# Kernel tuning notes

Hardware: AMD Instinct MI355X
Metric: run time of the kernel (lower is better)

## Reference

```python
import jax, jax.numpy as jnp
import numpy as np

EPS = 1e-5
NEG = -10000.0


def rel_shift(x):
    # x: [B, H, T1, T2] with T2 = 2*T1 - 1 -> returns [B, H, T1, T1]
    B, H, T1, T2 = x.shape
    x = jnp.pad(x, ((0, 0), (0, 0), (0, 0), (1, 0)))        # [B,H,T1,T2+1]
    x = x.reshape(B, H, T2 + 1, T1)[:, :, 1:, :].reshape(B, H, T1, T2)
    return x[:, :, :, : T2 // 2 + 1]


def setup_inputs() -> dict:
    key = jax.random.key(0)
    B, C, T, H = 4, 512, 1024, 8
    ks = jax.random.split(key, 16)
    s = 0.02
    inp = {
        "x": jax.random.normal(ks[0], (B, C, T), jnp.float32),
        "pos_emb": jax.random.normal(ks[1], (1, C, 2 * T - 1), jnp.float32),
        "x_mask": jnp.ones((B, 1, T), jnp.float32),
        "gamma": jnp.ones((C,), jnp.float32),
        "beta": jnp.zeros((C,), jnp.float32),
        "Wq": jax.random.normal(ks[2], (C, C), jnp.float32) * s,
        "bq": jnp.zeros((C,), jnp.float32),
        "Wk": jax.random.normal(ks[3], (C, C), jnp.float32) * s,
        "bk": jnp.zeros((C,), jnp.float32),
        "Wv": jax.random.normal(ks[4], (C, C), jnp.float32) * s,
        "bv": jnp.zeros((C,), jnp.float32),
        "Wp": jax.random.normal(ks[5], (C, C), jnp.float32) * s,
        "u_bias": jax.random.normal(ks[6], (H, C // H), jnp.float32) * s,
        "v_bias": jax.random.normal(ks[7], (H, C // H), jnp.float32) * s,
        "Wo": jax.random.normal(ks[8], (C, C), jnp.float32) * s,
        "bo": jnp.zeros((C,), jnp.float32),
    }
    return inp


def reference(x, pos_emb, x_mask, gamma, beta, Wq, bq, Wk, bk, Wv, bv, Wp,
              u_bias, v_bias, Wo, bo):
    B, C, T = x.shape
    H, Dh = u_bias.shape

    # channel LayerNorm (axis=1)
    mean = jnp.mean(x, axis=1, keepdims=True)
    var = jnp.mean((x - mean) ** 2, axis=1, keepdims=True)
    xn = (x - mean) * jax.lax.rsqrt(var + EPS)
    xn = xn * gamma[None, :, None] + beta[None, :, None]

    conv1x1 = lambda W, b, z: jnp.einsum('oc,bct->bot', W, z) + b[None, :, None]
    q = conv1x1(Wq, bq, xn).reshape(B, H, Dh, T)
    k = conv1x1(Wk, bk, xn).reshape(B, H, Dh, T)
    v = conv1x1(Wv, bv, xn).reshape(B, H, Dh, T)
    p = jnp.einsum('oc,xct->xot', Wp, pos_emb)          # [1, C, 2T-1], no bias
    p = p.reshape(p.shape[0], H, Dh, -1)[0]             # [H, Dh, 2T-1]

    content = jnp.einsum('bhdt,bhds->bhts', q + u_bias[None, :, :, None], k)
    pos = jnp.einsum('bhdt,hds->bhts', q + v_bias[None, :, :, None], p)
    pos = rel_shift(pos)                                 # [B, H, T, T]

    score = (content + pos) / jnp.sqrt(jnp.float32(C))
    attn_mask = x_mask[:, :, None, :] * x_mask[:, :, :, None]  # [B,1,T,T]
    score = jnp.where(attn_mask == 0, NEG, score)
    attn = jax.nn.softmax(score, axis=-1)

    # context[d,t] = sum_s v[d,s] * attn[s,t]
    ctx = jnp.einsum('bhds,bhst->bhdt', v, attn).reshape(B, C, T)
    return jnp.einsum('oc,bct->bot', Wo, ctx) + bo[None, :, None]
```

## Files before the change

kernel.cpp:

```cpp
#include <hip/hip_runtime.h>
#include <hip/hip_bf16.h>
#include <cmath>

typedef unsigned short u16;
typedef __bf16 bf16_t;
typedef bf16_t bf16x8 __attribute__((ext_vector_type(8)));
typedef bf16_t bf16x2 __attribute__((ext_vector_type(2)));
typedef float f32x4 __attribute__((ext_vector_type(4)));
typedef u16 u16x8 __attribute__((ext_vector_type(8)));

#define MFMA16(A,B,C) __builtin_amdgcn_mfma_f32_16x16x32_bf16(A,B,C,0,0,0)

#define CB 512
#define TT 1024
#define NH 8
#define DH 64
#define ALPHA (0.044194173824159216f * 1.4426950408889634f)
#define MASKL 14426.950408889634f

static __device__ __forceinline__ u16 f2b(float f) {
  union { bf16_t b; u16 u; } r; r.b = (bf16_t)f; return r.u;
}
static __device__ __forceinline__ unsigned cvt2(float lo, float hi) {
  union { bf16x2 v; unsigned u; } r;
  r.v[0] = (bf16_t)lo; r.v[1] = (bf16_t)hi; return r.u;
}
static __device__ __forceinline__ float b2f(u16 u) {
  return __uint_as_float(((unsigned)u) << 16);
}
static __device__ __forceinline__ bf16x8 ldb8(const u16* p) {
  return *reinterpret_cast<const bf16x8*>(p);
}

__global__ __launch_bounds__(256)
void prefix_kernel(const float* __restrict__ Wq, const float* __restrict__ Wk,
                   const float* __restrict__ Wv, const float* __restrict__ Wp,
                   const float* __restrict__ Wo,
                   u16* __restrict__ Wstk, u16* __restrict__ WoB,
                   const float* __restrict__ pe, u16* __restrict__ posT,
                   const float* __restrict__ x, const float* __restrict__ gamma,
                   const float* __restrict__ beta, u16* __restrict__ xnT)
{
  __shared__ float tile[64][65];
  const int bid = blockIdx.x;
  const int tid = threadIdx.x;
  if (bid < 640) {
    int i = bid * 256 + tid;
    int sel = i >> 15, loc = i & 32767;
    const float* src = (sel == 0) ? Wq : (sel == 1) ? Wk : (sel == 2) ? Wv
                     : (sel == 3) ? Wp : Wo;
    const float4 a = ((const float4*)src)[loc * 2 + 0];
    const float4 b = ((const float4*)src)[loc * 2 + 1];
    u16x8 o;
    o[0] = f2b(a.x); o[1] = f2b(a.y); o[2] = f2b(a.z); o[3] = f2b(a.w);
    o[4] = f2b(b.x); o[5] = f2b(b.y); o[6] = f2b(b.z); o[7] = f2b(b.w);
    u16* dst = (sel < 4) ? (Wstk + (size_t)i * 8) : (WoB + (size_t)loc * 8);
    *(u16x8*)dst = o;
  } else if (bid < 896) {
    int bb = bid - 640;
    int j0 = (bb & 31) * 64, c0 = (bb >> 5) * 64;
    for (int e = tid; e < 4096; e += 256) {
      int cc = e >> 6, jj = e & 63;
      int j = j0 + jj;
      tile[jj][cc] = (j < 2047) ? pe[(size_t)(c0 + cc) * 2047 + j] : 0.f;
    }
    __syncthreads();
    for (int e = tid; e < 4096; e += 256) {
      int jj = e >> 6, cc = e & 63;
      posT[(size_t)(j0 + jj) * 512 + c0 + cc] = f2b(tile[jj][cc]);
    }
  } else {
    float (*sred)[33]  = (float(*)[33])&tile[0][0];
    float (*ssred)[33] = (float(*)[33])&tile[8][0];
    int bb = bid - 896;
    int tl = tid & 31, cg = tid >> 5;
    int t = (bb & 31) * 32 + tl;
    int b = bb >> 5;
    const float* xb = x + (size_t)b * CB * TT + t;
    float s = 0.f, ss = 0.f;
    for (int c = cg * 64; c < cg * 64 + 64; ++c) {
      float v = xb[(size_t)c * TT];
      s += v; ss += v * v;
    }
    sred[cg][tl] = s; ssred[cg][tl] = ss;
    __syncthreads();
    float S = 0.f, SS = 0.f;
    #pragma unroll
    for (int g = 0; g < 8; ++g) { S += sred[g][tl]; SS += ssred[g][tl]; }
    float mean = S * (1.f / 512.f);
    float var = SS * (1.f / 512.f) - mean * mean;
    float rstd = rsqrtf(var + 1e-5f);
    u16* orow = xnT + ((size_t)b * TT + t) * CB;
    for (int c8 = 0; c8 < 8; ++c8) {
      int c = cg * 64 + c8 * 8;
      u16x8 o;
      #pragma unroll
      for (int j = 0; j < 8; ++j) {
        float v = xb[(size_t)(c + j) * TT];
        o[j] = f2b((v - mean) * rstd * gamma[c + j] + beta[c + j]);
      }
      *(u16x8*)(orow + c) = o;
    }
  }
}

__global__ __launch_bounds__(256)
void proj_kernel(const u16* __restrict__ Wstk, const u16* __restrict__ xnT,
                 const u16* __restrict__ posT,
                 const float* __restrict__ bq, const float* __restrict__ ub,
                 const float* __restrict__ bk, const float* __restrict__ bv,
                 u16* __restrict__ quB, u16* __restrict__ kB, u16* __restrict__ vB,
                 u16* __restrict__ pB)
{
  const int bid = blockIdx.x;
  const int tid = threadIdx.x, w = tid >> 6, lane = tid & 63;
  const int ln16 = lane & 15, kg = lane >> 4;
  if (bid < 768) {
    const int bx = bid & 7;
    const int t = bid >> 3;
    const int my = t % 24;
    const int z = t / 24;
    const int wm = w & 1, wn = w >> 1;
    const int sec = my >> 3;
    const int m0l = (my & 7) * 64 + wm * 32;
    const int n0 = bx * 128 + wn * 64;
    const long XS = (long)TT * CB;
    const long QS = (long)NH * TT * DH;
    const u16* Ar = Wstk + (size_t)(sec * 512 + m0l + ln16) * 512 + kg * 8;
    const u16* Br = xnT + (size_t)z * XS + (size_t)(n0 + ln16) * 512 + kg * 8;
    f32x4 acc[2][4] = {};
    #pragma unroll 2
    for (int ks = 0; ks < 16; ++ks) {
      bf16x8 a[2], bb[4];
      #pragma unroll
      for (int mt = 0; mt < 2; ++mt) a[mt] = ldb8(Ar + (size_t)mt * 16 * 512 + ks * 32);
      #pragma unroll
      for (int nt = 0; nt < 4; ++nt) bb[nt] = ldb8(Br + (size_t)nt * 16 * 512 + ks * 32);
      #pragma unroll
      for (int mt = 0; mt < 2; ++mt)
        #pragma unroll
        for (int nt = 0; nt < 4; ++nt)
          acc[mt][nt] = MFMA16(a[mt], bb[nt], acc[mt][nt]);
    }
    const float scl = (sec == 0) ? ALPHA : 1.f;
    float add[2][4];
    #pragma unroll
    for (int mt = 0; mt < 2; ++mt)
      #pragma unroll
      for (int jr = 0; jr < 4; ++jr) {
        int m = m0l + mt * 16 + kg * 4 + jr;
        add[mt][jr] = (sec == 0) ? (bq[m] + ub[m]) : (sec == 1) ? bk[m] : bv[m];
      }
    if (sec < 2) {
      u16* dst = sec ? kB : quB;
      #pragma unroll
      for (int mt = 0; mt < 2; ++mt)
        #pragma unroll
        for (int nt = 0; nt < 4; ++nt) {
          const int n = n0 + nt * 16 + ln16;
          const int m_low = m0l + mt * 16;
          const size_t o = (size_t)z * QS +
                           ((size_t)(m_low >> 6) * TT + n) * 64 + (m_low & 63) + kg * 4;
          uint2 o2;
          o2.x = cvt2((acc[mt][nt][0] + add[mt][0]) * scl,
                      (acc[mt][nt][1] + add[mt][1]) * scl);
          o2.y = cvt2((acc[mt][nt][2] + add[mt][2]) * scl,
                      (acc[mt][nt][3] + add[mt][3]) * scl);
          *reinterpret_cast<uint2*>(dst + o) = o2;
        }
    } else {
      #pragma unroll
      for (int mt = 0; mt < 2; ++mt)
        #pragma unroll
        for (int nt = 0; nt < 4; ++nt) {
          const int n = n0 + nt * 16 + ln16;
          #pragma unroll
          for (int jr = 0; jr < 4; ++jr)
            vB[(size_t)z * QS + (size_t)(m0l + mt * 16 + kg * 4 + jr) * TT + n] =
                f2b(acc[mt][nt][jr] + add[mt][jr]);
        }
    }
  } else {
    const int i = bid - 768;
    const int m0 = (i >> 5) * 64 + (w & 1) * 32;
    const int n0 = (i & 31) * 64 + (w >> 1) * 32;
    const u16* Ar = Wstk + (size_t)(1536 + m0 + ln16) * 512 + kg * 8;
    const u16* Br = posT + (size_t)(n0 + ln16) * 512 + kg * 8;
    f32x4 acc[2][2] = {};
    #pragma unroll 2
    for (int ks = 0; ks < 16; ++ks) {
      bf16x8 a[2], bb[2];
      #pragma unroll
      for (int mt = 0; mt < 2; ++mt) a[mt] = ldb8(Ar + (size_t)mt * 16 * 512 + ks * 32);
      #pragma unroll
      for (int nt = 0; nt < 2; ++nt) bb[nt] = ldb8(Br + (size_t)nt * 16 * 512 + ks * 32);
      #pragma unroll
      for (int mt = 0; mt < 2; ++mt)
        #pragma unroll
        for (int nt = 0; nt < 2; ++nt)
          acc[mt][nt] = MFMA16(a[mt], bb[nt], acc[mt][nt]);
    }
    #pragma unroll
    for (int mt = 0; mt < 2; ++mt)
      #pragma unroll
      for (int nt = 0; nt < 2; ++nt) {
        const int n = n0 + nt * 16 + ln16;
        const int m_low = m0 + mt * 16;
        const size_t o = ((size_t)(m_low >> 6) * 2048 + n) * 64 + (m_low & 63) + kg * 4;
        uint2 o2;
        o2.x = cvt2(acc[mt][nt][0], acc[mt][nt][1]);
        o2.y = cvt2(acc[mt][nt][2], acc[mt][nt][3]);
        *reinterpret_cast<uint2*>(pB + o) = o2;
      }
  }
}

template<int K, int OMODE>
__global__ __launch_bounds__(256)
void gemm2(const u16* __restrict__ A, const u16* __restrict__ XT,
           long xStride, long oStride, int Nout,
           const float* __restrict__ b0, void* __restrict__ outv)
{
  const int tid = threadIdx.x, w = tid >> 6, lane = tid & 63;
  const int ln16 = lane & 15, kg = lane >> 4;
  const int wm = w & 1, wn = w >> 1;
  const int m0 = blockIdx.y * 64 + wm * 32;
  const int n0 = blockIdx.x * 128 + wn * 64;
  const int z = blockIdx.z;
  const u16* Ar = A + (size_t)(m0 + ln16) * K + kg * 8;
  const u16* Br = XT + (size_t)z * xStride + (size_t)(n0 + ln16) * K + kg * 8;
  f32x4 acc[2][4] = {};
  #pragma unroll 2
  for (int ks = 0; ks < K / 32; ++ks) {
    bf16x8 a[2], bb[4];
    #pragma unroll
    for (int mt = 0; mt < 2; ++mt) a[mt] = ldb8(Ar + (size_t)mt * 16 * K + ks * 32);
    #pragma unroll
    for (int nt = 0; nt < 4; ++nt) bb[nt] = ldb8(Br + (size_t)nt * 16 * K + ks * 32);
    #pragma unroll
    for (int mt = 0; mt < 2; ++mt)
      #pragma unroll
      for (int nt = 0; nt < 4; ++nt)
        acc[mt][nt] = MFMA16(a[mt], bb[nt], acc[mt][nt]);
  }
  float add[2][4];
  #pragma unroll
  for (int mt = 0; mt < 2; ++mt)
    #pragma unroll
    for (int jr = 0; jr < 4; ++jr)
      add[mt][jr] = b0 ? b0[m0 + mt * 16 + kg * 4 + jr] : 0.f;
  #pragma unroll
  for (int mt = 0; mt < 2; ++mt)
    #pragma unroll
    for (int nt = 0; nt < 4; ++nt) {
      const int n = n0 + nt * 16 + ln16;
      if constexpr (OMODE == 0) {
        float* out = (float*)outv;
        #pragma unroll
        for (int jr = 0; jr < 4; ++jr)
          out[(size_t)z * oStride + (size_t)(m0 + mt * 16 + kg * 4 + jr) * Nout + n] =
              acc[mt][nt][jr] + add[mt][jr];
      } else {
        const int m_low = m0 + mt * 16;
        const size_t o = (size_t)z * oStride +
                         ((size_t)(m_low >> 6) * Nout + n) * 64 + (m_low & 63) + kg * 4;
        uint2 o2;
        o2.x = cvt2(acc[mt][nt][0] + add[mt][0], acc[mt][nt][1] + add[mt][1]);
        o2.y = cvt2(acc[mt][nt][2] + add[mt][2], acc[mt][nt][3] + add[mt][3]);
        *reinterpret_cast<uint2*>((u16*)outv + o) = o2;
      }
    }
}

__global__ __launch_bounds__(256)
void corr_kernel(const u16* __restrict__ pp, const float* __restrict__ ub,
                 const float* __restrict__ vb, float* __restrict__ corr)
{
  const int h = blockIdx.y;
  const int j = blockIdx.x * 256 + threadIdx.x;
  __shared__ float dl[64];
  if (threadIdx.x < 64)
    dl[threadIdx.x] = vb[h * 64 + threadIdx.x] - ub[h * 64 + threadIdx.x];
  __syncthreads();
  const u16* prow = pp + ((size_t)h * 2048 + j) * 64;
  float s = 0.f;
  #pragma unroll
  for (int d8 = 0; d8 < 8; ++d8) {
    union { bf16x8 v; u16 u[8]; } pu;
    pu.v = ldb8(prow + d8 * 8);
    #pragma unroll
    for (int e = 0; e < 8; ++e) s += b2f(pu.u[e]) * dl[d8 * 8 + e];
  }
  corr[h * 2048 + j] = s * ALPHA;
}

__global__ __launch_bounds__(256)
void stats_mfma(const u16* __restrict__ qu, const u16* __restrict__ kk_,
                const u16* __restrict__ pp, const float* __restrict__ corr,
                const float* __restrict__ xmask, float* __restrict__ ls)
{
  const int tid = threadIdx.x;
  const int w = tid >> 6, lane = tid & 63;
  const int ln16 = lane & 15, kg = lane >> 4;
  const int bid = blockIdx.x;
  const int bh = (bid & 7) + 8 * ((bid >> 3) & 3);
  const int rest = bid >> 5;
  const int qi0 = (rest & 31) * 32;
  const int part = rest >> 5;
  const int b = bh >> 3, h = bh & 7;
  const u16* quP = qu + (size_t)bh * TT * DH;
  const u16* kP  = kk_ + (size_t)bh * TT * DH;
  const u16* pP  = pp + (size_t)h * 2048 * DH;
  const float* corrP = corr + (h << 11);

  __shared__ u16 G[4][32][100];
  __shared__ float red[4][32];

  bf16x8 qa[2][2];
  #pragma unroll
  for (int mt = 0; mt < 2; ++mt)
    #pragma unroll
    for (int kc = 0; kc < 2; ++kc)
      qa[mt][kc] = ldb8(&quP[(size_t)(qi0 + mt * 16 + ln16) * DH + kc * 32 + kg * 8]);
  float aq[2][4];
  #pragma unroll
  for (int mt = 0; mt < 2; ++mt)
    #pragma unroll
    for (int jr = 0; jr < 4; ++jr)
      aq[mt][jr] = (xmask[b * TT + qi0 + mt * 16 + kg * 4 + jr] - 1.f) * MASKL;

  float rs[2][4] = {};
  for (int c = 0; c < 2; ++c) {
    const int ki0 = (part * 8 + c * 4 + w) * 64;
    const int j0 = ki0 - qi0 + 992;
    #pragma unroll
    for (int nt = 0; nt < 6; ++nt) {
      const size_t po = (size_t)(j0 + nt * 16 + ln16) * DH + kg * 8;
      bf16x8 pb0 = ldb8(&pP[po]);
      bf16x8 pb1 = ldb8(&pP[po + 32]);
      const float cval = corrP[j0 + nt * 16 + ln16];
      #pragma unroll
      for (int mt = 0; mt < 2; ++mt) {
        f32x4 g = {0.f, 0.f, 0.f, 0.f};
        g = MFMA16(qa[mt][0], pb0, g);
        g = MFMA16(qa[mt][1], pb1, g);
        #pragma unroll
        for (int jr = 0; jr < 4; ++jr)
          G[w][mt * 16 + kg * 4 + jr][nt * 16 + ln16] = f2b(g[jr] + cval);
      }
    }
    #pragma unroll
    for (int nt = 0; nt < 4; ++nt) {
      const size_t ko = (size_t)(ki0 + nt * 16 + ln16) * DH + kg * 8;
      bf16x8 kb0 = ldb8(&kP[ko]);
      bf16x8 kb1 = ldb8(&kP[ko + 32]);
      const float ak = (xmask[b * TT + ki0 + nt * 16 + ln16] - 1.f) * MASKL;
      #pragma unroll
      for (int mt = 0; mt < 2; ++mt) {
        f32x4 dd = { aq[mt][0] + ak, aq[mt][1] + ak, aq[mt][2] + ak, aq[mt][3] + ak };
        dd = MFMA16(qa[mt][0], kb0, dd);
        dd = MFMA16(qa[mt][1], kb1, dd);
        #pragma unroll
        for (int jr = 0; jr < 4; ++jr) {
          const int qrow = mt * 16 + kg * 4 + jr;
          const int u = nt * 16 + ln16 - qrow + 31;
          rs[mt][jr] += exp2f(dd[jr] + b2f(G[w][qrow][u]));
        }
      }
    }
  }
  #pragma unroll
  for (int mt = 0; mt < 2; ++mt)
    #pragma unroll
    for (int jr = 0; jr < 4; ++jr) {
      float v = rs[mt][jr];
      v += __shfl_xor(v, 1); v += __shfl_xor(v, 2);
      v += __shfl_xor(v, 4); v += __shfl_xor(v, 8);
      rs[mt][jr] = v;
    }
  if (ln16 == 0) {
    #pragma unroll
    for (int mt = 0; mt < 2; ++mt)
      #pragma unroll
      for (int jr = 0; jr < 4; ++jr)
        red[w][mt * 16 + kg * 4 + jr] = rs[mt][jr];
  }
  __syncthreads();
  if (tid < 32)
    ls[(size_t)part * 32768 + (size_t)bh * TT + qi0 + tid] =
        red[0][tid] + red[1][tid] + red[2][tid] + red[3][tid];
}

__global__ __launch_bounds__(256)
void ctx_mfma(const u16* __restrict__ qu, const u16* __restrict__ kk_,
              const u16* __restrict__ vv, const u16* __restrict__ pp,
              const float* __restrict__ corr, const float* __restrict__ xmask,
              u16* __restrict__ ctx2)
{
  const int tid = threadIdx.x;
  const int w = tid >> 6, lane = tid & 63;
  const int ln16 = lane & 15, kg = lane >> 4;
  const int l48 = lane & 48;
  const int bid = blockIdx.x;
  const int bh = (bid & 7) + 8 * ((bid >> 3) & 3);
  const int rest = bid >> 5;
  const int t0 = (rest & 15) * 64;
  const int part = rest >> 4;
  const int b = bh >> 3, h = bh & 7;
  const u16* quP = qu + (size_t)bh * TT * DH;
  const u16* kP  = kk_ + (size_t)bh * TT * DH;
  const u16* vP  = vv + (size_t)bh * DH * TT;
  const u16* pP  = pp + (size_t)h * 2048 * DH;
  const float* corrP = corr + (h << 11);

  __shared__ __align__(16) u16 P[2][64][72];

  bf16x8 ka[4][2];
  #pragma unroll
  for (int nt = 0; nt < 4; ++nt)
    #pragma unroll
    for (int kc = 0; kc < 2; ++kc)
      ka[nt][kc] = ldb8(&kP[(size_t)(t0 + nt * 16 + ln16) * DH + kc * 32 + kg * 8]);
  float at4[4];
  #pragma unroll
  for (int nt = 0; nt < 4; ++nt)
    at4[nt] = (xmask[b * TT + t0 + nt * 16 + ln16] - 1.f) * MASKL;

  auto scores = [&](int qcn, int buf) {
    const int qw = qcn * 64 + w * 16;
    const int j0 = t0 - qw + 1008;
    const size_t qo = (size_t)(qw + ln16) * DH + kg * 8;
    bf16x8 qa0 = ldb8(&quP[qo]), qa1 = ldb8(&quP[qo + 32]);
    f32x4 g[5];
    #pragma unroll
    for (int n = 0; n < 5; ++n) {
      const size_t po = (size_t)(j0 + n * 16 + ln16) * DH + kg * 8;
      bf16x8 pb0 = ldb8(&pP[po]), pb1 = ldb8(&pP[po + 32]);
      const float cval = corrP[j0 + n * 16 + ln16];
      f32x4 t = {cval, cval, cval, cval};
      t = MFMA16(qa0, pb0, t);
      t = MFMA16(qa1, pb1, t);
      g[n] = t;
    }
    float sg[4][5];
    #pragma unroll
    for (int jr = 0; jr < 4; ++jr) {
      const int qrow = kg * 4 + jr;
      const int src = l48 | ((ln16 + 15 - qrow) & 15);
      #pragma unroll
      for (int n = 0; n < 5; ++n) sg[jr][n] = __shfl(g[n][jr], src);
    }
    float aqv[4];
    #pragma unroll
    for (int jr = 0; jr < 4; ++jr)
      aqv[jr] = (xmask[b * TT + qw + kg * 4 + jr] - 1.f) * MASKL;
    #pragma unroll
    for (int nt = 0; nt < 4; ++nt) {
      f32x4 dd = { aqv[0] + at4[nt], aqv[1] + at4[nt],
                   aqv[2] + at4[nt], aqv[3] + at4[nt] };
      dd = MFMA16(qa0, ka[nt][0], dd);
      dd = MFMA16(qa1, ka[nt][1], dd);
      float ev[4];
      #pragma unroll
      for (int jr = 0; jr < 4; ++jr) {
        const int qrow = kg * 4 + jr;
        const float val = (ln16 <= qrow) ? sg[jr][nt] : sg[jr][nt + 1];
        ev[jr] = exp2f(dd[jr] + val);
      }
      uint2 o2;
      o2.x = cvt2(ev[0], ev[1]);
      o2.y = cvt2(ev[2], ev[3]);
      *reinterpret_cast<uint2*>(&P[buf][nt * 16 + ln16][w * 16 + kg * 4]) = o2;
    }
  };

  f32x4 cacc[4] = {};
  scores(part * 4, 0);
  __syncthreads();
  #pragma unroll
  for (int i = 0; i < 4; ++i) {
    const int qc = part * 4 + i;
    const size_t vbase = (size_t)(w * 16 + ln16) * TT + qc * 64 + kg * 8;
    bf16x8 vf0 = ldb8(&vP[vbase]), vf1 = ldb8(&vP[vbase + 32]);
    __builtin_amdgcn_s_setprio(1);
    #pragma unroll
    for (int nt = 0; nt < 4; ++nt) {
      bf16x8 pb0 = *reinterpret_cast<const bf16x8*>(&P[i & 1][nt * 16 + ln16][kg * 8]);
      bf16x8 pb1 = *reinterpret_cast<const bf16x8*>(&P[i & 1][nt * 16 + ln16][32 + kg * 8]);
      cacc[nt] = MFMA16(vf0, pb0, cacc[nt]);
      cacc[nt] = MFMA16(vf1, pb1, cacc[nt]);
    }
    __builtin_amdgcn_s_setprio(0);
    if (i < 3) {
      scores(qc + 1, (i + 1) & 1);
      __syncthreads();
    }
  }
  #pragma unroll
  for (int nt = 0; nt < 4; ++nt) {
    const int t = t0 + nt * 16 + ln16;
    uint2 o2;
    o2.x = cvt2(cacc[nt][0], cacc[nt][1]);
    o2.y = cvt2(cacc[nt][2], cacc[nt][3]);
    *reinterpret_cast<uint2*>(
      &ctx2[((size_t)b * TT + t) * 2048 + part * 512 + h * 64 + w * 16 + kg * 4]) = o2;
  }
}

__global__ __launch_bounds__(256)
void vscale(u16* __restrict__ vv, const float* __restrict__ ls)
{
  int i = blockIdx.x * 256 + threadIdx.x;
  int bh = i >> 13;
  int rem = i & 8191;
  int d = rem >> 7;
  int qi0 = (rem & 127) * 8;
  const float* lsP = ls + bh * 1024 + qi0;
  u16* row = vv + ((size_t)bh * 64 + d) * 1024 + qi0;
  union { u16x8 v; u16 u[8]; } t;
  t.v = *(u16x8*)row;
  u16x8 o;
  #pragma unroll
  for (int e = 0; e < 8; ++e) {
    float linv = __builtin_amdgcn_rcpf(lsP[e] + lsP[32768 + e]);
    o[e] = f2b(b2f(t.u[e]) * linv);
  }
  *(u16x8*)row = o;
}

__global__ __launch_bounds__(256)
void reduce_ctx(const u16* __restrict__ ctx2, u16* __restrict__ ctxS)
{
  int i = blockIdx.x * 256 + threadIdx.x;
  int row = i >> 6;
  int c0 = (i & 63) * 8;
  const u16* src = ctx2 + (size_t)row * 2048 + c0;
  float s[8] = {};
  #pragma unroll
  for (int p = 0; p < 4; ++p) {
    union { u16x8 v; u16 u[8]; } t;
    t.v = *(const u16x8*)(src + p * 512);
    #pragma unroll
    for (int e = 0; e < 8; ++e) s[e] += b2f(t.u[e]);
  }
  u16x8 o;
  #pragma unroll
  for (int e = 0; e < 8; ++e) o[e] = f2b(s[e]);
  *(u16x8*)(ctxS + (size_t)row * 512 + c0) = o;
}

extern "C" void kernel_launch(void* const* d_in, const int* in_sizes, int n_in,
                              void* d_out, int out_size, void* d_ws, size_t ws_size,
                              hipStream_t stream)
{
  (void)in_sizes; (void)n_in; (void)out_size;
  const float* x     = (const float*)d_in[0];
  const float* pe    = (const float*)d_in[1];
  const float* xm    = (const float*)d_in[2];
  const float* gamma = (const float*)d_in[3];
  const float* beta  = (const float*)d_in[4];
  const float* Wq    = (const float*)d_in[5];
  const float* bq    = (const float*)d_in[6];
  const float* Wk    = (const float*)d_in[7];
  const float* bk    = (const float*)d_in[8];
  const float* Wv    = (const float*)d_in[9];
  const float* bv    = (const float*)d_in[10];
  const float* Wp    = (const float*)d_in[11];
  const float* ub    = (const float*)d_in[12];
  const float* vb    = (const float*)d_in[13];
  const float* Wo    = (const float*)d_in[14];
  const float* bo    = (const float*)d_in[15];

  char* ws = (char*)d_ws;
  u16*  quB  = (u16*) (ws + 0);
  u16*  ctxS = (u16*) (ws + 0);
  u16*  kB   = (u16*) (ws + 4194304);
  u16*  vB   = (u16*) (ws + 8388608);
  u16*  pB   = (u16*) (ws + 12582912);
  float* corrB = (float*)(ws + 14680064);
  float* lsB = (float*)(ws + 14745600);
  u16*  WoB  = (u16*) (ws + 15007744);
  u16*  ctx2 = (u16*) (ws + 15532032);
  u16*  xnT  = (u16*) (ws + 15532032);
  u16*  posT = (u16*) (ws + 19726336);
  u16*  Wstk = (u16*) (ws + 21823488);
  if (ws_size < 32309248) return;

  dim3 blk(256);

  prefix_kernel<<<dim3(1024), blk, 0, stream>>>(
      Wq, Wk, Wv, Wp, Wo, Wstk, WoB, pe, posT, x, gamma, beta, xnT);
  proj_kernel<<<dim3(1024), blk, 0, stream>>>(
      Wstk, xnT, posT, bq, ub, bk, bv, quB, kB, vB, pB);
  corr_kernel<<<dim3(8, 8), blk, 0, stream>>>(pB, ub, vb, corrB);

  stats_mfma<<<dim3(2048), blk, 0, stream>>>(quB, kB, pB, corrB, xm, lsB);
  vscale<<<dim3(1024), blk, 0, stream>>>(vB, lsB);
  ctx_mfma<<<dim3(2048), blk, 0, stream>>>(quB, kB, vB, pB, corrB, xm, ctx2);
  reduce_ctx<<<dim3(1024), blk, 0, stream>>>(ctx2, ctxS);

  gemm2<512, 0><<<dim3(8, 8, 4), blk, 0, stream>>>(
      WoB, ctxS, (long)TT * CB, (long)CB * TT, TT, bo, (float*)d_out);
}
```

Before: 198.6 us.

## Fold corr kernel into prefix/proj and keep P in registers for ctx MFMA

The standalone corr kernel goes away. A new prefix block precomputes Wp^T(v_bias-u_bias) per head, and extra proj blocks dot posT rows with it to produce the correction vector, which saves one launch. ctx_mfma no longer stages exp scores through double-buffered LDS with barriers. Each wave feeds its score fragments straight into 16x16x16 MFMAs against V fragments for all 64 head dims, and the four waves' partial sums are reduced through LDS at the end. This trades per-chunk syncs for 4x more accumulators, a final cross-wave reduction and a changed rounding order of the correction term.

Result: slower. 229.1 us (+15.3%).

```diff
diff --git a/kernel.cpp b/kernel.cpp
--- a/kernel.cpp
+++ b/kernel.cpp
@@ -8,8 +8,10 @@
 typedef bf16_t bf16x2 __attribute__((ext_vector_type(2)));
 typedef float f32x4 __attribute__((ext_vector_type(4)));
 typedef u16 u16x8 __attribute__((ext_vector_type(8)));
+typedef short s16x4 __attribute__((ext_vector_type(4)));
 
 #define MFMA16(A,B,C) __builtin_amdgcn_mfma_f32_16x16x32_bf16(A,B,C,0,0,0)
+#define MFMA16K16(A,B,C) __builtin_amdgcn_mfma_f32_16x16x16bf16_1k(A,B,C,0,0,0)
 
 #define CB 512
 #define TT 1024
@@ -39,7 +41,9 @@
                    u16* __restrict__ Wstk, u16* __restrict__ WoB,
                    const float* __restrict__ pe, u16* __restrict__ posT,
                    const float* __restrict__ x, const float* __restrict__ gamma,
-                   const float* __restrict__ beta, u16* __restrict__ xnT)
+                   const float* __restrict__ beta, u16* __restrict__ xnT,
+                   const float* __restrict__ ub, const float* __restrict__ vb,
+                   float* __restrict__ wcorr)
 {
   __shared__ float tile[64][65];
   const int bid = blockIdx.x;
@@ -69,7 +73,7 @@
       int jj = e >> 6, cc = e & 63;
       posT[(size_t)(j0 + jj) * 512 + c0 + cc] = f2b(tile[jj][cc]);
     }
-  } else {
+  } else if (bid < 1024) {
     float (*sred)[33]  = (float(*)[33])&tile[0][0];
     float (*ssred)[33] = (float(*)[33])&tile[8][0];
     int bb = bid - 896;
@@ -101,6 +105,21 @@
       }
       *(u16x8*)(orow + c) = o;
     }
+  } else {
+    float* dl2 = &tile[0][0];
+    for (int i = tid; i < 512; i += 256) dl2[i] = vb[i] - ub[i];
+    __syncthreads();
+    const int hh = tid >> 5;
+    const int c0 = (tid & 31) * 16;
+    float acc[16] = {};
+    for (int d = 0; d < 64; ++d) {
+      const float dv = dl2[hh * 64 + d];
+      const float* wrow = Wp + (size_t)(hh * 64 + d) * 512 + c0;
+      #pragma unroll
+      for (int j = 0; j < 16; ++j) acc[j] += dv * wrow[j];
+    }
+    #pragma unroll
+    for (int j = 0; j < 16; ++j) wcorr[hh * 512 + c0 + j] = acc[j];
   }
 }
 
@@ -109,9 +128,11 @@
                  const u16* __restrict__ posT,
                  const float* __restrict__ bq, const float* __restrict__ ub,
                  const float* __restrict__ bk, const float* __restrict__ bv,
+                 const float* __restrict__ wcorr,
                  u16* __restrict__ quB, u16* __restrict__ kB, u16* __restrict__ vB,
-                 u16* __restrict__ pB)
-{
+                 u16* __restrict__ pB, float* __restrict__ corrOut)
+{
+  __shared__ float wc[512];
   const int bid = blockIdx.x;
   const int tid = threadIdx.x, w = tid >> 6, lane = tid & 63;
   const int ln16 = lane & 15, kg = lane >> 4;
@@ -180,7 +201,7 @@
                 f2b(acc[mt][nt][jr] + add[mt][jr]);
         }
     }
-  } else {
+  } else if (bid < 1024) {
     const int i = bid - 768;
     const int m0 = (i >> 5) * 64 + (w & 1) * 32;
     const int n0 = (i & 31) * 64 + (w >> 1) * 32;
@@ -212,6 +233,22 @@
         o2.y = cvt2(acc[mt][nt][2], acc[mt][nt][3]);
         *reinterpret_cast<uint2*>(pB + o) = o2;
       }
+  } else {
+    const int i = bid - 1024;
+    const int hh = i >> 3;
+    const int j = (i & 7) * 256 + tid;
+    for (int c = tid; c < 512; c += 256) wc[c] = wcorr[hh * 512 + c];
+    __syncthreads();
+    const u16* prow = posT + (size_t)j * 512;
+    float s = 0.f;
+    #pragma unroll 4
+    for (int c8 = 0; c8 < 64; ++c8) {
+      union { bf16x8 v; u16 u[8]; } pu;
+      pu.v = ldb8(prow + c8 * 8);
+      #pragma unroll
+      for (int e = 0; e < 8; ++e) s += b2f(pu.u[e]) * wc[c8 * 8 + e];
+    }
+    corrOut[hh * 2048 + j] = s * ALPHA;
   }
 }
 
@@ -270,28 +307,6 @@
         *reinterpret_cast<uint2*>((u16*)outv + o) = o2;
       }
     }
-}
-
-__global__ __launch_bounds__(256)
-void corr_kernel(const u16* __restrict__ pp, const float* __restrict__ ub,
-                 const float* __restrict__ vb, float* __restrict__ corr)
-{
-  const int h = blockIdx.y;
-  const int j = blockIdx.x * 256 + threadIdx.x;
-  __shared__ float dl[64];
-  if (threadIdx.x < 64)
-    dl[threadIdx.x] = vb[h * 64 + threadIdx.x] - ub[h * 64 + threadIdx.x];
-  __syncthreads();
-  const u16* prow = pp + ((size_t)h * 2048 + j) * 64;
-  float s = 0.f;
-  #pragma unroll
-  for (int d8 = 0; d8 < 8; ++d8) {
-    union { bf16x8 v; u16 u[8]; } pu;
-    pu.v = ldb8(prow + d8 * 8);
-    #pragma unroll
-    for (int e = 0; e < 8; ++e) s += b2f(pu.u[e]) * dl[d8 * 8 + e];
-  }
-  corr[h * 2048 + j] = s * ALPHA;
 }
 
 __global__ __launch_bounds__(256)
@@ -413,7 +428,7 @@
   const u16* pP  = pp + (size_t)h * 2048 * DH;
   const float* corrP = corr + (h << 11);
 
-  __shared__ __align__(16) u16 P[2][64][72];
+  __shared__ float buf[4][2][64][4][4];
 
   bf16x8 ka[4][2];
   #pragma unroll
@@ -426,29 +441,31 @@
   for (int nt = 0; nt < 4; ++nt)
     at4[nt] = (xmask[b * TT + t0 + nt * 16 + ln16] - 1.f) * MASKL;
 
-  auto scores = [&](int qcn, int buf) {
-    const int qw = qcn * 64 + w * 16;
+  f32x4 cacc[4][4] = {};
+  for (int qc = part * 4; qc < part * 4 + 4; ++qc) {
+    const int qw = qc * 64 + w * 16;
     const int j0 = t0 - qw + 1008;
     const size_t qo = (size_t)(qw + ln16) * DH + kg * 8;
     bf16x8 qa0 = ldb8(&quP[qo]), qa1 = ldb8(&quP[qo + 32]);
-    f32x4 g[5];
+    s16x4 vfr[4];
+    #pragma unroll
+    for (int df = 0; df < 4; ++df)
+      vfr[df] = *reinterpret_cast<const s16x4*>(
+          &vP[(size_t)(df * 16 + ln16) * TT + qw + kg * 4]);
+    float sg[4][5];
     #pragma unroll
     for (int n = 0; n < 5; ++n) {
       const size_t po = (size_t)(j0 + n * 16 + ln16) * DH + kg * 8;
       bf16x8 pb0 = ldb8(&pP[po]), pb1 = ldb8(&pP[po + 32]);
       const float cval = corrP[j0 + n * 16 + ln16];
-      f32x4 t = {cval, cval, cval, cval};
-      t = MFMA16(qa0, pb0, t);
-      t = MFMA16(qa1, pb1, t);
-      g[n] = t;
-    }
-    float sg[4][5];
-    #pragma unroll
-    for (int jr = 0; jr < 4; ++jr) {
-      const int qrow = kg * 4 + jr;
-      const int src = l48 | ((ln16 + 15 - qrow) & 15);
-      #pragma unroll
-      for (int n = 0; n < 5; ++n) sg[jr][n] = __shfl(g[n][jr], src);
+      f32x4 g = {cval, cval, cval, cval};
+      g = MFMA16(qa0, pb0, g);
+      g = MFMA16(qa1, pb1, g);
+      #pragma unroll
+      for (int jr = 0; jr < 4; ++jr) {
+        const int src = l48 | ((ln16 + 15 - (kg * 4 + jr)) & 15);
+        sg[jr][n] = __shfl(g[jr], src);
+      }
     }
     float aqv[4];
     #pragma unroll
@@ -467,43 +484,44 @@
         const float val = (ln16 <= qrow) ? sg[jr][nt] : sg[jr][nt + 1];
         ev[jr] = exp2f(dd[jr] + val);
       }
-      uint2 o2;
-      o2.x = cvt2(ev[0], ev[1]);
-      o2.y = cvt2(ev[2], ev[3]);
-      *reinterpret_cast<uint2*>(&P[buf][nt * 16 + ln16][w * 16 + kg * 4]) = o2;
-    }
-  };
-
-  f32x4 cacc[4] = {};
-  scores(part * 4, 0);
-  __syncthreads();
-  #pragma unroll
-  for (int i = 0; i < 4; ++i) {
-    const int qc = part * 4 + i;
-    const size_t vbase = (size_t)(w * 16 + ln16) * TT + qc * 64 + kg * 8;
-    bf16x8 vf0 = ldb8(&vP[vbase]), vf1 = ldb8(&vP[vbase + 32]);
-    __builtin_amdgcn_s_setprio(1);
-    #pragma unroll
-    for (int nt = 0; nt < 4; ++nt) {
-      bf16x8 pb0 = *reinterpret_cast<const bf16x8*>(&P[i & 1][nt * 16 + ln16][kg * 8]);
-      bf16x8 pb1 = *reinterpret_cast<const bf16x8*>(&P[i & 1][nt * 16 + ln16][32 + kg * 8]);
-      cacc[nt] = MFMA16(vf0, pb0, cacc[nt]);
-      cacc[nt] = MFMA16(vf1, pb1, cacc[nt]);
-    }
-    __builtin_amdgcn_s_setprio(0);
-    if (i < 3) {
-      scores(qc + 1, (i + 1) & 1);
-      __syncthreads();
-    }
-  }
-  #pragma unroll
-  for (int nt = 0; nt < 4; ++nt) {
-    const int t = t0 + nt * 16 + ln16;
-    uint2 o2;
-    o2.x = cvt2(cacc[nt][0], cacc[nt][1]);
-    o2.y = cvt2(cacc[nt][2], cacc[nt][3]);
-    *reinterpret_cast<uint2*>(
-      &ctx2[((size_t)b * TT + t) * 2048 + part * 512 + h * 64 + w * 16 + kg * 4]) = o2;
+      union { uint2 u; s16x4 s; } pa;
+      pa.u = make_uint2(cvt2(ev[0], ev[1]), cvt2(ev[2], ev[3]));
+      #pragma unroll
+      for (int df = 0; df < 4; ++df)
+        cacc[df][nt] = MFMA16K16(vfr[df], pa.s, cacc[df][nt]);
+    }
+  }
+  #pragma unroll
+  for (int r = 0; r < 2; ++r) {
+    if (r) __syncthreads();
+    #pragma unroll
+    for (int y = 0; y < 2; ++y)
+      #pragma unroll
+      for (int nt = 0; nt < 4; ++nt)
+        #pragma unroll
+        for (int jr = 0; jr < 4; ++jr)
+          buf[w][y][lane][nt][jr] = cacc[r * 2 + y][nt][jr];
+    __syncthreads();
+    if (w < 2) {
+      const int df = r * 2 + w;
+      #pragma unroll
+      for (int nt = 0; nt < 4; ++nt) {
+        float s0 = buf[0][w][lane][nt][0] + buf[1][w][lane][nt][0] +
+                   buf[2][w][lane][nt][0] + buf[3][w][lane][nt][0];
+        float s1 = buf[0][w][lane][nt][1] + buf[1][w][lane][nt][1] +
+                   buf[2][w][lane][nt][1] + buf[3][w][lane][nt][1];
+        float s2 = buf[0][w][lane][nt][2] + buf[1][w][lane][nt][2] +
+                   buf[2][w][lane][nt][2] + buf[3][w][lane][nt][2];
+        float s3 = buf[0][w][lane][nt][3] + buf[1][w][lane][nt][3] +
+                   buf[2][w][lane][nt][3] + buf[3][w][lane][nt][3];
+        const int t = t0 + nt * 16 + ln16;
+        uint2 o2;
+        o2.x = cvt2(s0, s1);
+        o2.y = cvt2(s2, s3);
+        *reinterpret_cast<uint2*>(
+          &ctx2[((size_t)b * TT + t) * 2048 + part * 512 + h * 64 + df * 16 + kg * 4]) = o2;
+      }
+    }
   }
 }
 
@@ -584,15 +602,15 @@
   u16*  xnT  = (u16*) (ws + 15532032);
   u16*  posT = (u16*) (ws + 19726336);
   u16*  Wstk = (u16*) (ws + 21823488);
+  float* wcorrB = (float*)(ws + 23920640);
   if (ws_size < 32309248) return;
 
   dim3 blk(256);
 
-  prefix_kernel<<<dim3(1024), blk, 0, stream>>>(
-      Wq, Wk, Wv, Wp, Wo, Wstk, WoB, pe, posT, x, gamma, beta, xnT);
-  proj_kernel<<<dim3(1024), blk, 0, stream>>>(
-      Wstk, xnT, posT, bq, ub, bk, bv, quB, kB, vB, pB);
-  corr_kernel<<<dim3(8, 8), blk, 0, stream>>>(pB, ub, vb, corrB);
+  prefix_kernel<<<dim3(1025), blk, 0, stream>>>(
+      Wq, Wk, Wv, Wp, Wo, Wstk, WoB, pe, posT, x, gamma, beta, xnT, ub, vb, wcorrB);
+  proj_kernel<<<dim3(1088), blk, 0, stream>>>(
+      Wstk, xnT, posT, bq, ub, bk, bv, wcorrB, quB, kB, vB, pB, corrB);
 
   stats_mfma<<<dim3(2048), blk, 0, stream>>>(quB, kB, pB, corrB, xm, lsB);
   vscale<<<dim3(1024), blk, 0, stream>>>(vB, lsB);
```

## Fold corr into prefix/proj kernels and drop split-K context reduction

Applied to the files above, without the earlier changes.

The positional-bias correction is now computed algebraically: a prefix block folds (v_bias - u_bias) into Wp to form per-head weight vectors, and extra proj_kernel blocks dot those vectors with posT. This removes the separate corr_kernel launch. ctx_mfma no longer splits the key range into four parts. Each block now loops over all 16 key chunks and writes ctxS directly, which eliminates the ctx2 buffer and the reduce_ctx kernel. The trade-off is only 512 ctx blocks instead of 2048, with longer serial loops, so occupancy and parallelism drop on a chip with many CUs.

Result: no change. 201.9 us (+1.6%).

```diff
diff --git a/kernel.cpp b/kernel.cpp
--- a/kernel.cpp
+++ b/kernel.cpp
@@ -39,7 +39,9 @@
                    u16* __restrict__ Wstk, u16* __restrict__ WoB,
                    const float* __restrict__ pe, u16* __restrict__ posT,
                    const float* __restrict__ x, const float* __restrict__ gamma,
-                   const float* __restrict__ beta, u16* __restrict__ xnT)
+                   const float* __restrict__ beta, u16* __restrict__ xnT,
+                   const float* __restrict__ ub, const float* __restrict__ vb,
+                   float* __restrict__ wcorr)
 {
   __shared__ float tile[64][65];
   const int bid = blockIdx.x;
@@ -69,7 +71,7 @@
       int jj = e >> 6, cc = e & 63;
       posT[(size_t)(j0 + jj) * 512 + c0 + cc] = f2b(tile[jj][cc]);
     }
-  } else {
+  } else if (bid < 1024) {
     float (*sred)[33]  = (float(*)[33])&tile[0][0];
     float (*ssred)[33] = (float(*)[33])&tile[8][0];
     int bb = bid - 896;
@@ -101,6 +103,21 @@
       }
       *(u16x8*)(orow + c) = o;
     }
+  } else {
+    float* dl2 = &tile[0][0];
+    for (int i = tid; i < 512; i += 256) dl2[i] = vb[i] - ub[i];
+    __syncthreads();
+    const int hh = tid >> 5;
+    const int c0 = (tid & 31) * 16;
+    float acc[16] = {};
+    for (int d = 0; d < 64; ++d) {
+      const float dv = dl2[hh * 64 + d];
+      const float* wrow = Wp + (size_t)(hh * 64 + d) * 512 + c0;
+      #pragma unroll
+      for (int j = 0; j < 16; ++j) acc[j] += dv * wrow[j];
+    }
+    #pragma unroll
+    for (int j = 0; j < 16; ++j) wcorr[hh * 512 + c0 + j] = acc[j];
   }
 }
 
@@ -109,9 +126,11 @@
                  const u16* __restrict__ posT,
                  const float* __restrict__ bq, const float* __restrict__ ub,
                  const float* __restrict__ bk, const float* __restrict__ bv,
+                 const float* __restrict__ wcorr,
                  u16* __restrict__ quB, u16* __restrict__ kB, u16* __restrict__ vB,
-                 u16* __restrict__ pB)
-{
+                 u16* __restrict__ pB, float* __restrict__ corrOut)
+{
+  __shared__ float wc[512];
   const int bid = blockIdx.x;
   const int tid = threadIdx.x, w = tid >> 6, lane = tid & 63;
   const int ln16 = lane & 15, kg = lane >> 4;
@@ -180,7 +199,7 @@
                 f2b(acc[mt][nt][jr] + add[mt][jr]);
         }
     }
-  } else {
+  } else if (bid < 1024) {
     const int i = bid - 768;
     const int m0 = (i >> 5) * 64 + (w & 1) * 32;
     const int n0 = (i & 31) * 64 + (w >> 1) * 32;
@@ -212,6 +231,22 @@
         o2.y = cvt2(acc[mt][nt][2], acc[mt][nt][3]);
         *reinterpret_cast<uint2*>(pB + o) = o2;
       }
+  } else {
+    const int i = bid - 1024;
+    const int hh = i >> 3;
+    const int j = (i & 7) * 256 + tid;
+    for (int c = tid; c < 512; c += 256) wc[c] = wcorr[hh * 512 + c];
+    __syncthreads();
+    const u16* prow = posT + (size_t)j * 512;
+    float s = 0.f;
+    #pragma unroll 4
+    for (int c8 = 0; c8 < 64; ++c8) {
+      union { bf16x8 v; u16 u[8]; } pu;
+      pu.v = ldb8(prow + c8 * 8);
+      #pragma unroll
+      for (int e = 0; e < 8; ++e) s += b2f(pu.u[e]) * wc[c8 * 8 + e];
+    }
+    corrOut[hh * 2048 + j] = s * ALPHA;
   }
 }
 
@@ -270,28 +305,6 @@
         *reinterpret_cast<uint2*>((u16*)outv + o) = o2;
       }
     }
-}
-
-__global__ __launch_bounds__(256)
-void corr_kernel(const u16* __restrict__ pp, const float* __restrict__ ub,
-                 const float* __restrict__ vb, float* __restrict__ corr)
-{
-  const int h = blockIdx.y;
-  const int j = blockIdx.x * 256 + threadIdx.x;
-  __shared__ float dl[64];
-  if (threadIdx.x < 64)
-    dl[threadIdx.x] = vb[h * 64 + threadIdx.x] - ub[h * 64 + threadIdx.x];
-  __syncthreads();
-  const u16* prow = pp + ((size_t)h * 2048 + j) * 64;
-  float s = 0.f;
-  #pragma unroll
-  for (int d8 = 0; d8 < 8; ++d8) {
-    union { bf16x8 v; u16 u[8]; } pu;
-    pu.v = ldb8(prow + d8 * 8);
-    #pragma unroll
-    for (int e = 0; e < 8; ++e) s += b2f(pu.u[e]) * dl[d8 * 8 + e];
-  }
-  corr[h * 2048 + j] = s * ALPHA;
 }
 
 __global__ __launch_bounds__(256)
@@ -395,7 +408,7 @@
 void ctx_mfma(const u16* __restrict__ qu, const u16* __restrict__ kk_,
               const u16* __restrict__ vv, const u16* __restrict__ pp,
               const float* __restrict__ corr, const float* __restrict__ xmask,
-              u16* __restrict__ ctx2)
+              u16* __restrict__ ctxS)
 {
   const int tid = threadIdx.x;
   const int w = tid >> 6, lane = tid & 63;
@@ -403,9 +416,7 @@
   const int l48 = lane & 48;
   const int bid = blockIdx.x;
   const int bh = (bid & 7) + 8 * ((bid >> 3) & 3);
-  const int rest = bid >> 5;
-  const int t0 = (rest & 15) * 64;
-  const int part = rest >> 4;
+  const int t0 = (bid >> 5) * 64;
   const int b = bh >> 3, h = bh & 7;
   const u16* quP = qu + (size_t)bh * TT * DH;
   const u16* kP  = kk_ + (size_t)bh * TT * DH;
@@ -475,12 +486,10 @@
   };
 
   f32x4 cacc[4] = {};
-  scores(part * 4, 0);
+  scores(0, 0);
   __syncthreads();
-  #pragma unroll
-  for (int i = 0; i < 4; ++i) {
-    const int qc = part * 4 + i;
-    const size_t vbase = (size_t)(w * 16 + ln16) * TT + qc * 64 + kg * 8;
+  for (int i = 0; i < 16; ++i) {
+    const size_t vbase = (size_t)(w * 16 + ln16) * TT + i * 64 + kg * 8;
     bf16x8 vf0 = ldb8(&vP[vbase]), vf1 = ldb8(&vP[vbase + 32]);
     __builtin_amdgcn_s_setprio(1);
     #pragma unroll
@@ -491,8 +500,8 @@
       cacc[nt] = MFMA16(vf1, pb1, cacc[nt]);
     }
     __builtin_amdgcn_s_setprio(0);
-    if (i < 3) {
-      scores(qc + 1, (i + 1) & 1);
+    if (i < 15) {
+      scores(i + 1, (i + 1) & 1);
       __syncthreads();
     }
   }
@@ -503,7 +512,7 @@
     o2.x = cvt2(cacc[nt][0], cacc[nt][1]);
     o2.y = cvt2(cacc[nt][2], cacc[nt][3]);
     *reinterpret_cast<uint2*>(
-      &ctx2[((size_t)b * TT + t) * 2048 + part * 512 + h * 64 + w * 16 + kg * 4]) = o2;
+      &ctxS[((size_t)b * TT + t) * 512 + h * 64 + w * 16 + kg * 4]) = o2;
   }
 }
 
@@ -526,27 +535,6 @@
     o[e] = f2b(b2f(t.u[e]) * linv);
   }
   *(u16x8*)row = o;
-}
-
-__global__ __launch_bounds__(256)
-void reduce_ctx(const u16* __restrict__ ctx2, u16* __restrict__ ctxS)
-{
-  int i = blockIdx.x * 256 + threadIdx.x;
-  int row = i >> 6;
-  int c0 = (i & 63) * 8;
-  const u16* src = ctx2 + (size_t)row * 2048 + c0;
-  float s[8] = {};
-  #pragma unroll
-  for (int p = 0; p < 4; ++p) {
-    union { u16x8 v; u16 u[8]; } t;
-    t.v = *(const u16x8*)(src + p * 512);
-    #pragma unroll
-    for (int e = 0; e < 8; ++e) s[e] += b2f(t.u[e]);
-  }
-  u16x8 o;
-  #pragma unroll
-  for (int e = 0; e < 8; ++e) o[e] = f2b(s[e]);
-  *(u16x8*)(ctxS + (size_t)row * 512 + c0) = o;
 }
 
 extern "C" void kernel_launch(void* const* d_in, const int* in_sizes, int n_in,
@@ -573,31 +561,29 @@
 
   char* ws = (char*)d_ws;
   u16*  quB  = (u16*) (ws + 0);
-  u16*  ctxS = (u16*) (ws + 0);
   u16*  kB   = (u16*) (ws + 4194304);
   u16*  vB   = (u16*) (ws + 8388608);
   u16*  pB   = (u16*) (ws + 12582912);
   float* corrB = (float*)(ws + 14680064);
   float* lsB = (float*)(ws + 14745600);
   u16*  WoB  = (u16*) (ws + 15007744);
-  u16*  ctx2 = (u16*) (ws + 15532032);
+  u16*  ctxS = (u16*) (ws + 15532032);
   u16*  xnT  = (u16*) (ws + 15532032);
   u16*  posT = (u16*) (ws + 19726336);
   u16*  Wstk = (u16*) (ws + 21823488);
+  float* wcorrB = (float*)(ws + 23920640);
   if (ws_size < 32309248) return;
 
   dim3 blk(256);
 
-  prefix_kernel<<<dim3(1024), blk, 0, stream>>>(
-      Wq, Wk, Wv, Wp, Wo, Wstk, WoB, pe, posT, x, gamma, beta, xnT);
-  proj_kernel<<<dim3(1024), blk, 0, stream>>>(
-      Wstk, xnT, posT, bq, ub, bk, bv, quB, kB, vB, pB);
-  corr_kernel<<<dim3(8, 8), blk, 0, stream>>>(pB, ub, vb, corrB);
+  prefix_kernel<<<dim3(1025), blk, 0, stream>>>(
+      Wq, Wk, Wv, Wp, Wo, Wstk, WoB, pe, posT, x, gamma, beta, xnT, ub, vb, wcorrB);
+  proj_kernel<<<dim3(1088), blk, 0, stream>>>(
+      Wstk, xnT, posT, bq, ub, bk, bv, wcorrB, quB, kB, vB, pB, corrB);
 
   stats_mfma<<<dim3(2048), blk, 0, stream>>>(quB, kB, pB, corrB, xm, lsB);
   vscale<<<dim3(1024), blk, 0, stream>>>(vB, lsB);
-  ctx_mfma<<<dim3(2048), blk, 0, stream>>>(quB, kB, vB, pB, corrB, xm, ctx2);
-  reduce_ctx<<<dim3(1024), blk, 0, stream>>>(ctx2, ctxS);
+  ctx_mfma<<<dim3(512), blk, 0, stream>>>(quB, kB, vB, pB, corrB, xm, ctxS);
 
   gemm2<512, 0><<<dim3(8, 8, 4), blk, 0, stream>>>(
       WoB, ctxS, (long)TT * CB, (long)CB * TT, TT, bo, (float*)d_out);
```
